# Optimization experiments

Hardware: AMD Instinct MI355X
Metric: run time of the kernel (lower is better)

Reference implementation:

```python
import math
import jax, jax.numpy as jnp
import numpy as np

HID, NHEADS, MEM, LIM = 1024, 16, 512, 2048
HEAD = HID // NHEADS  # 64


def _skew(X, pad_value):
    # shift row m right by m steps: [B, M, L] -> [B, M, M+L]
    B, M, L = X.shape
    X = jnp.pad(X, ((0, 0), (0, 0), (0, M + 1)), constant_values=pad_value)
    X = X.reshape(B, -1)[:, :-M]
    return X.reshape(B, M, M + L)


def _unskew(X):
    # reverse of _skew: [B, M, M+L] -> [B, M, L]
    B, M, LM = X.shape
    L = LM - M
    X = jnp.pad(X.reshape(B, -1), ((0, 0), (0, M)))
    return X.reshape(B, M, LM + 1)[:, :, :L]


def _heads(x):
    # [B, S, K*D] -> [B*K, S, D]
    B, S, _ = x.shape
    return x.reshape(B, S, NHEADS, HEAD).transpose(0, 2, 1, 3).reshape(B * NHEADS, S, HEAD)


def setup_inputs() -> dict:
    key = jax.random.key(0)
    ks = jax.random.split(key, 8)
    B = 8
    s = 1.0 / math.sqrt(HID)
    return {
        "query": jax.random.normal(ks[0], (B, MEM, HID), jnp.float32),
        "key": jax.random.normal(ks[1], (B, MEM + LIM, HID), jnp.float32),
        "value": jax.random.normal(ks[2], (B, MEM + LIM, HID), jnp.float32),
        "key_pe": jax.random.normal(ks[3], (1, HEAD, LIM), jnp.float32),
        "Wq": jax.random.normal(ks[4], (HID, HID), jnp.float32) * s,
        "Wk": jax.random.normal(ks[5], (HID, HID), jnp.float32) * s,
        "Wv": jax.random.normal(ks[6], (HID, HID), jnp.float32) * s,
        "Wo": jax.random.normal(ks[7], (HID, HID), jnp.float32) * s,
    }


def reference(query, key, value, key_pe, Wq, Wk, Wv, Wo):
    B = query.shape[0]
    q = _heads(query @ Wq.T)   # [B*K, M, D]
    k = _heads(key @ Wk.T)     # [B*K, M+L, D]
    v = _heads(value @ Wv.T)   # [B*K, M+L, D]
    # content term via skew/unskew trick
    attn_cont = _unskew(jnp.einsum('bmd,bnd->bmn', q, k))  # [B*K, M, L]
    # relative-position term
    attn_pos = jnp.einsum('bmd,dl->bml', q, key_pe[0])     # [B*K, M, L]
    attn = jax.nn.softmax((attn_cont + attn_pos) / math.sqrt(HEAD), axis=-1)
    out = jnp.matmul(_skew(attn, 0.0), v)                  # [B*K, M, D]
    out = out.reshape(B, NHEADS, MEM, HEAD).transpose(0, 2, 1, 3).reshape(B, MEM, HID)
    return out @ Wo.T
```

## Files before the change

kernel.cpp:

```cpp
#include <hip/hip_runtime.h>
#include <hip/hip_bf16.h>
#include <stdint.h>


typedef __attribute__((ext_vector_type(8))) __bf16 bfrag;
typedef __attribute__((ext_vector_type(4))) float f4;

#define DEVFN static __device__ __forceinline__

DEVFN void glds16(const void* g, void* l) {
  __builtin_amdgcn_global_load_lds((const __attribute__((address_space(1))) void*)g,
                                   (__attribute__((address_space(3))) void*)l, 16, 0, 0);
}

DEVFN bfrag cvt8(const float* p) {
  f4 a = *(const f4*)p;
  f4 b = *(const f4*)(p + 4);
  bfrag v;
  v[0] = (__bf16)a.x; v[1] = (__bf16)a.y; v[2] = (__bf16)a.z; v[3] = (__bf16)a.w;
  v[4] = (__bf16)b.x; v[5] = (__bf16)b.y; v[6] = (__bf16)b.z; v[7] = (__bf16)b.w;
  return v;
}

__global__ __launch_bounds__(256) void conv4(const float* __restrict__ a0, const float* __restrict__ a1,
                                             const float* __restrict__ a2, const float* __restrict__ a3,
                                             __bf16* __restrict__ d0, __bf16* __restrict__ d1,
                                             __bf16* __restrict__ d2, __bf16* __restrict__ d3) {
  int bx = blockIdx.x;
  int sel = bx >> 9;
  const float* s = sel == 0 ? a0 : sel == 1 ? a1 : sel == 2 ? a2 : a3;
  __bf16* d = sel == 0 ? d0 : sel == 1 ? d1 : sel == 2 ? d2 : d3;
  int i = ((bx & 511) * 256 + (int)threadIdx.x) * 8;
  *(bfrag*)(d + i) = cvt8(s + i);
}

__global__ __launch_bounds__(256) void convin(const float* __restrict__ q, const float* __restrict__ k,
                                              const float* __restrict__ v,
                                              __bf16* __restrict__ qd, __bf16* __restrict__ kd,
                                              __bf16* __restrict__ vd) {
  int bx = blockIdx.x;
  const float* s; __bf16* d; int lb;
  if (bx < 2048)       { s = q; d = qd; lb = bx; }
  else if (bx < 12288) { s = k; d = kd; lb = bx - 2048; }
  else                 { s = v; d = vd; lb = bx - 12288; }
  int i = (lb * 256 + (int)threadIdx.x) * 8;
  *(bfrag*)(d + i) = cvt8(s + i);
}

__global__ __launch_bounds__(256) void pek(const float* __restrict__ pe,
                                           __bf16* __restrict__ peT) {
  int i = blockIdx.x * 256 + threadIdx.x;
  if (i < 64 * 2048) {
    int d = i >> 11, l = i & 2047;
    peT[(size_t)(l + 64) * 64 + d] = (__bf16)pe[i];
  } else {
    int zi = i - 64 * 2048;
    int row = zi >> 6, dd = zi & 63;
    int r = row < 64 ? row : (2112 + row - 64);
    peT[(size_t)r * 64 + dd] = (__bf16)0.f;
  }
}

DEVFN bfrag rdfrag(const __bf16* L, int row, int kc, int g) {
  return *(const bfrag*)&L[row * 64 + (((g + 4 * kc) ^ (row & 7)) << 3)];
}

DEVFN void core16(const __bf16* __restrict__ A, const __bf16* __restrict__ B,
                  __bf16* AL, __bf16* BL, f4 (&acc)[4][4],
                  int tid, int wr, int wc, int g, int cl) {
  auto stageA = [&](int s, int k0) {
#pragma unroll
    for (int j = 0; j < 4; ++j) {
      int slot = j * 256 + tid;
      int row = slot >> 3, ch = slot & 7;
      glds16(A + (size_t)row * 1024 + k0 + ((ch ^ (row & 7)) << 3),
             &AL[s * 8192 + (slot << 3)]);
    }
  };
  auto stageB = [&](int k0) {
#pragma unroll
    for (int j = 0; j < 4; ++j) {
      int slot = j * 256 + tid;
      int row = slot >> 3, ch = slot & 7;
      glds16(B + (size_t)row * 1024 + k0 + ((ch ^ (row & 7)) << 3),
             &BL[slot << 3]);
    }
  };

  stageA(0, 0);
  for (int kt = 0; kt < 16; ++kt) {
    const int s = kt & 1;
    stageB(kt * 64);
    if (kt < 15) {
      stageA(s ^ 1, (kt + 1) * 64);
      asm volatile("s_waitcnt vmcnt(4)" ::: "memory");
    } else {
      asm volatile("s_waitcnt vmcnt(0)" ::: "memory");
    }
    __builtin_amdgcn_s_barrier();
    const __bf16* As = &AL[s * 8192];
#pragma unroll
    for (int kc = 0; kc < 2; ++kc) {
      bfrag af[4], bf[4];
#pragma unroll
      for (int i = 0; i < 4; ++i) {
        af[i] = rdfrag(As, 64 * wr + 16 * i + cl, kc, g);
        bf[i] = rdfrag(BL, 64 * wc + 16 * i + cl, kc, g);
      }
      __builtin_amdgcn_s_setprio(1);
#pragma unroll
      for (int am = 0; am < 4; ++am)
#pragma unroll
        for (int bn = 0; bn < 4; ++bn)
          acc[am][bn] =
              __builtin_amdgcn_mfma_f32_16x16x32_bf16(af[am], bf[bn], acc[am][bn], 0, 0, 0);
      __builtin_amdgcn_s_setprio(0);
    }
    __builtin_amdgcn_s_barrier();
  }
}

__global__ __launch_bounds__(256) void projk_c(const __bf16* __restrict__ Aq, const __bf16* __restrict__ Ak,
                                               const __bf16* __restrict__ Av,
                                               const __bf16* __restrict__ Wqb, const __bf16* __restrict__ Wkb,
                                               const __bf16* __restrict__ Wvb,
                                               __bf16* __restrict__ qws, __bf16* __restrict__ kws,
                                               __bf16* __restrict__ vtws) {
  __shared__ alignas(16) __bf16 AL[2 * 128 * 64];
  __shared__ alignas(16) __bf16 BL[128 * 64];
  int bx = blockIdx.x;
  const __bf16* A; const __bf16* B; __bf16* C; int nb, lb, rpb, trans;
  if (bx < 256)       { A = Aq; B = Wqb; C = qws;  lb = bx;        nb = 256;  rpb = 4;  trans = 0; }
  else if (bx < 1536) { A = Ak; B = Wkb; C = kws;  lb = bx - 256;  nb = 1280; rpb = 20; trans = 0; }
  else                { A = Av; B = Wvb; C = vtws; lb = bx - 1536; nb = 1280; rpb = 20; trans = 1; }

  const int tid = threadIdx.x;
  const int lane = tid & 63, wv = tid >> 6;
  const int wr = wv >> 1, wc = wv & 1;
  const int g = lane >> 4, cl = lane & 15;

  int v = (lb & 7) * (nb >> 3) + (lb >> 3);
  const int trow = v >> 3;
  const int r0 = trow * 128, c0 = (v & 7) * 128;

  f4 acc[4][4] = {};
  core16(A + (size_t)r0 * 1024, B + (size_t)c0 * 1024, AL, BL, acc,
         tid, wr, wc, g, cl);

  int Sseq = rpb << 7;
  int b = trow / rpb;
  int sbase = r0 - b * Sseq;
#pragma unroll
  for (int am = 0; am < 4; ++am)
#pragma unroll
    for (int bn = 0; bn < 4; ++bn) {
      int jg = c0 + 64 * wc + 16 * bn + cl;
      int h = jg >> 6, d = jg & 63;
#pragma unroll
      for (int r = 0; r < 4; ++r) {
        int s = sbase + 64 * wr + 16 * am + 4 * g + r;
        size_t dst = trans ? ((size_t)(b * 16 + h) * 64 + d) * 2560 + s
                           : ((size_t)(b * 16 + h) * Sseq + s) * 64 + d;
        C[dst] = (__bf16)acc[am][bn][r];
      }
    }
}

DEVFN void stageA_row(const float* ap, __bf16* lds, int arow, int ahalf) {
  const f4* p = (const f4*)ap;
#pragma unroll
  for (int q = 0; q < 4; ++q) {
    f4 a = p[2 * q], b = p[2 * q + 1];
    bfrag v;
    v[0] = (__bf16)a.x; v[1] = (__bf16)a.y; v[2] = (__bf16)a.z; v[3] = (__bf16)a.w;
    v[4] = (__bf16)b.x; v[5] = (__bf16)b.y; v[6] = (__bf16)b.z; v[7] = (__bf16)b.w;
    int ch = (4 * ahalf + q) ^ (arow & 7);
    *(bfrag*)&lds[arow * 64 + ch * 8] = v;
  }
}

__global__ __launch_bounds__(256) void projk_f32(const float* __restrict__ Aq, const float* __restrict__ Ak,
                                                 const float* __restrict__ Av,
                                                 const __bf16* __restrict__ Wqb, const __bf16* __restrict__ Wkb,
                                                 const __bf16* __restrict__ Wvb,
                                                 __bf16* __restrict__ qws, __bf16* __restrict__ kws,
                                                 __bf16* __restrict__ vtws) {
  __shared__ alignas(16) __bf16 Alds[128 * 64];
  __shared__ alignas(16) __bf16 Blds[128 * 64];
  int bx = blockIdx.x;
  const float* A; const __bf16* B; __bf16* C; int nb, lb, rpb, trans;
  if (bx < 256)       { A = Aq; B = Wqb; C = qws;  lb = bx;        nb = 256;  rpb = 4;  trans = 0; }
  else if (bx < 1536) { A = Ak; B = Wkb; C = kws;  lb = bx - 256;  nb = 1280; rpb = 20; trans = 0; }
  else                { A = Av; B = Wvb; C = vtws; lb = bx - 1536; nb = 1280; rpb = 20; trans = 1; }

  const int tid = threadIdx.x;
  const int lane = tid & 63, wv = tid >> 6;
  const int wr = wv >> 1, wc = wv & 1;
  const int g = lane >> 4, cl = lane & 15;

  int v = (lb & 7) * (nb >> 3) + (lb >> 3);
  const int trow = v >> 3;
  const int r0 = trow * 128, c0 = (v & 7) * 128;

  f4 acc[4][4] = {};

  for (int k0 = 0; k0 < 1024; k0 += 64) {
    __syncthreads();
#pragma unroll
    for (int i = 0; i < 4; ++i) {
      int slot = tid + 256 * i;
      int row = slot >> 3, ch = slot & 7;
      glds16(B + (size_t)(c0 + row) * 1024 + k0 + ((ch ^ (row & 7)) << 3),
             &Blds[slot << 3]);
    }
    stageA_row(A + (size_t)(r0 + (tid >> 1)) * 1024 + k0 + (tid & 1) * 32,
               Alds, tid >> 1, tid & 1);
    __syncthreads();
#pragma unroll
    for (int kc = 0; kc < 2; ++kc) {
      bfrag af[4], bfv[4];
#pragma unroll
      for (int i = 0; i < 4; ++i) {
        int rA = 64 * wr + 16 * i + cl;
        af[i] = *(const bfrag*)&Alds[rA * 64 + (((g + 4 * kc) ^ (rA & 7)) << 3)];
        int rB = 64 * wc + 16 * i + cl;
        bfv[i] = *(const bfrag*)&Blds[rB * 64 + (((g + 4 * kc) ^ (rB & 7)) << 3)];
      }
#pragma unroll
      for (int am = 0; am < 4; ++am)
#pragma unroll
        for (int bn = 0; bn < 4; ++bn)
          acc[am][bn] =
              __builtin_amdgcn_mfma_f32_16x16x32_bf16(af[am], bfv[bn], acc[am][bn], 0, 0, 0);
    }
  }

  int Sseq = rpb << 7;
  int b = trow / rpb;
  int sbase = r0 - b * Sseq;
#pragma unroll
  for (int am = 0; am < 4; ++am)
#pragma unroll
    for (int bn = 0; bn < 4; ++bn) {
      int jg = c0 + 64 * wc + 16 * bn + cl;
      int h = jg >> 6, d = jg & 63;
#pragma unroll
      for (int r = 0; r < 4; ++r) {
        int s = sbase + 64 * wr + 16 * am + 4 * g + r;
        size_t dst = trans ? ((size_t)(b * 16 + h) * 64 + d) * 2560 + s
                           : ((size_t)(b * 16 + h) * Sseq + s) * 64 + d;
        C[dst] = (__bf16)acc[am][bn][r];
      }
    }
}

__global__ __launch_bounds__(256) void gemm_out(const __bf16* __restrict__ A,
                                                const __bf16* __restrict__ B,
                                                float* __restrict__ C) {
  __shared__ alignas(16) __bf16 AL[2 * 128 * 64];
  __shared__ alignas(16) __bf16 BL[128 * 64];
  const int tid = threadIdx.x;
  const int lane = tid & 63, wv = tid >> 6;
  const int wr = wv >> 1, wc = wv & 1;
  const int g = lane >> 4, cl = lane & 15;

  int bx = blockIdx.x;
  int v = (bx & 7) * 32 + (bx >> 3);
  const int r0 = (v >> 3) * 128, c0 = (v & 7) * 128;

  f4 acc[4][4] = {};
  core16(A + (size_t)r0 * 1024, B + (size_t)c0 * 1024, AL, BL, acc,
         tid, wr, wc, g, cl);

#pragma unroll
  for (int am = 0; am < 4; ++am)
#pragma unroll
    for (int bn = 0; bn < 4; ++bn)
#pragma unroll
      for (int r = 0; r < 4; ++r) {
        int rg = r0 + 64 * wr + 16 * am + 4 * g + r;
        int jg = c0 + 64 * wc + 16 * bn + cl;
        C[(size_t)rg * 1024 + jg] = acc[am][bn][r];
      }
}

#define SCL 0.18033688011112042f
#define FMX 20.0f

__global__ __launch_bounds__(256) void attnk(const __bf16* __restrict__ qws,
                                             const __bf16* __restrict__ kws,
                                             const __bf16* __restrict__ vtws,
                                             const __bf16* __restrict__ pews,
                                             __bf16* __restrict__ obuf) {
  __shared__ alignas(16) __bf16 Ks[64 * 64];
  __shared__ alignas(16) __bf16 QVs[64 * 64];
  __shared__ alignas(16) __bf16 PPs[64 * 64];
  __shared__ alignas(16) __bf16 Pbs[64 * 128];

  int bx = blockIdx.x;
  int vv = (bx & 7) * 128 + (bx >> 3);
  int bh = vv >> 3, mt = vv & 7;
  int m0 = mt * 64;
  const __bf16* qb = qws + (size_t)bh * 512 * 64;
  const __bf16* kb = kws + (size_t)bh * 2560 * 64;
  const __bf16* vb = vtws + (size_t)bh * 64 * 2560;

  const int tid = threadIdx.x;
  const int lane = tid & 63, w = tid >> 6;
  const int g = lane >> 4, cl = lane & 15;

#pragma unroll
  for (int i = 0; i < 2; ++i) {
    int slot = tid + 256 * i;
    int row = slot >> 3, ch = slot & 7;
    glds16(qb + (size_t)(m0 + row) * 64 + ((ch ^ (row & 7)) << 3), &QVs[slot << 3]);
  }
  __syncthreads();
  bfrag qf_all[4][2];
#pragma unroll
  for (int rb = 0; rb < 4; ++rb) {
    int rq = 16 * rb + cl;
#pragma unroll
    for (int kc = 0; kc < 2; ++kc)
      qf_all[rb][kc] = *(const bfrag*)&QVs[rq * 64 + (((g + 4 * kc) ^ (rq & 7)) << 3)];
  }

  f4 o[4] = {};
  float lsum[4] = {};

  for (int t = 0; t < 33; ++t) {
    int n0 = m0 + 64 * t;
    __syncthreads();
#pragma unroll
    for (int i = 0; i < 2; ++i) {
      int slot = tid + 256 * i;
      int row = slot >> 3, ch = slot & 7;
      glds16(kb + (size_t)(n0 + row) * 64 + ((ch ^ (row & 7)) << 3), &Ks[slot << 3]);
      glds16(vb + (size_t)row * 2560 + n0 + ((ch ^ (row & 7)) << 3), &QVs[slot << 3]);
      glds16(pews + (size_t)(64 * (t + 1) + row) * 64 + ((ch ^ (row & 7)) << 3),
             &PPs[slot << 3]);
    }
    __syncthreads();

    f4 sc[4] = {};
    __builtin_amdgcn_s_setprio(1);
#pragma unroll
    for (int kc = 0; kc < 2; ++kc)
#pragma unroll
      for (int cb = 0; cb < 4; ++cb) {
        int rk = 16 * cb + cl;
        bfrag kf = *(const bfrag*)&Ks[rk * 64 + (((g + 4 * kc) ^ (rk & 7)) << 3)];
        sc[cb] = __builtin_amdgcn_mfma_f32_16x16x32_bf16(qf_all[w][kc], kf, sc[cb], 0, 0, 0);
      }
    f4 pbacc[4] = {};
#pragma unroll
    for (int kc = 0; kc < 2; ++kc) {
      int rp = 16 * w + cl;
      bfrag pf = *(const bfrag*)&PPs[rp * 64 + (((g + 4 * kc) ^ (rp & 7)) << 3)];
#pragma unroll
      for (int rb = 0; rb < 4; ++rb)
        pbacc[rb] = __builtin_amdgcn_mfma_f32_16x16x32_bf16(qf_all[rb][kc], pf, pbacc[rb], 0, 0, 0);
    }
    __builtin_amdgcn_s_setprio(0);
    {
      int half = (t & 1) << 6;
      int c2 = 16 * w + cl;
#pragma unroll
      for (int rb = 0; rb < 4; ++rb)
#pragma unroll
        for (int r = 0; r < 4; ++r)
          Pbs[(16 * rb + 4 * g + r) * 128 + half + c2] = (__bf16)pbacc[rb][r];
    }
    __syncthreads();

    bool edge = (t == 0) || (t == 32);
#pragma unroll
    for (int r = 0; r < 4; ++r) {
      int jm = 16 * w + 4 * g + r;
#pragma unroll
      for (int cb = 0; cb < 4; ++cb) {
        int jn = 16 * cb + cl;
        int l = 64 * t + jn - jm;
        float pv = (float)Pbs[jm * 128 + (l & 127)];
        float ex = fmaf(sc[cb][r] + pv, SCL, -FMX);
        if (edge) ex = ((unsigned)l < 2048u) ? ex : -1e30f;
        float p = __builtin_amdgcn_exp2f(ex);
        lsum[r] += p;
        PPs[jm * 64 + (((jn >> 3) ^ (jm & 7)) << 3) + (jn & 7)] = (__bf16)p;
      }
    }

    __builtin_amdgcn_s_setprio(1);
#pragma unroll
    for (int kc = 0; kc < 2; ++kc) {
      int rp2 = 16 * w + cl;
      bfrag pa = *(const bfrag*)&PPs[rp2 * 64 + (((g + 4 * kc) ^ (rp2 & 7)) << 3)];
#pragma unroll
      for (int cb = 0; cb < 4; ++cb) {
        int rv = 16 * cb + cl;
        bfrag vf = *(const bfrag*)&QVs[rv * 64 + (((g + 4 * kc) ^ (rv & 7)) << 3)];
        o[cb] = __builtin_amdgcn_mfma_f32_16x16x32_bf16(pa, vf, o[cb], 0, 0, 0);
      }
    }
    __builtin_amdgcn_s_setprio(0);
  }

#pragma unroll
  for (int r = 0; r < 4; ++r)
#pragma unroll
    for (int off = 1; off < 16; off <<= 1) lsum[r] += __shfl_xor(lsum[r], off);

  int b = bh >> 4, h = bh & 15;
#pragma unroll
  for (int cb = 0; cb < 4; ++cb)
#pragma unroll
    for (int r = 0; r < 4; ++r) {
      int m = m0 + 16 * w + 4 * g + r;
      int d = 16 * cb + cl;
      obuf[((size_t)(b * 512 + m)) * 1024 + h * 64 + d] = (__bf16)(o[cb][r] / lsum[r]);
    }
}

extern "C" void kernel_launch(void* const* d_in, const int* in_sizes, int n_in,
                              void* d_out, int out_size, void* d_ws, size_t ws_size,
                              hipStream_t stream) {
  const float* query = (const float*)d_in[0];
  const float* key   = (const float*)d_in[1];
  const float* value = (const float*)d_in[2];
  const float* keype = (const float*)d_in[3];
  const float* Wq    = (const float*)d_in[4];
  const float* Wk    = (const float*)d_in[5];
  const float* Wv    = (const float*)d_in[6];
  const float* Wo    = (const float*)d_in[7];
  float* out = (float*)d_out;
  (void)in_sizes; (void)n_in; (void)out_size;

  char* ws = (char*)d_ws;
  size_t off = 0;
  auto alloc = [&](size_t bytes) {
    void* p = ws + off;
    off += (bytes + 255) & ~(size_t)255;
    return p;
  };
  __bf16* Wqb  = (__bf16*)alloc((size_t)1024 * 1024 * 2);
  __bf16* Wkb  = (__bf16*)alloc((size_t)1024 * 1024 * 2);
  __bf16* Wvb  = (__bf16*)alloc((size_t)1024 * 1024 * 2);
  __bf16* Wob  = (__bf16*)alloc((size_t)1024 * 1024 * 2);
  __bf16* peT  = (__bf16*)alloc((size_t)2176 * 64 * 2);
  __bf16* qws  = (__bf16*)alloc((size_t)128 * 512 * 64 * 2);
  __bf16* kws  = (__bf16*)alloc((size_t)128 * 2560 * 64 * 2);
  __bf16* vtws = (__bf16*)alloc((size_t)128 * 2560 * 64 * 2);

  const size_t NEED = (size_t)194 * 1024 * 1024;
  bool big = ws_size >= NEED;

  conv4<<<2048, 256, 0, stream>>>(Wq, Wk, Wv, Wo, Wqb, Wkb, Wvb, Wob);
  pek<<<544, 256, 0, stream>>>(keype, peT);

  __bf16* obuf;
  if (big) {
    __bf16* qbf = (__bf16*)alloc((size_t)8 * 512 * 1024 * 2);
    __bf16* kbf = (__bf16*)alloc((size_t)8 * 2560 * 1024 * 2);
    __bf16* vbf = (__bf16*)alloc((size_t)8 * 2560 * 1024 * 2);
    obuf = qbf;
    convin<<<22528, 256, 0, stream>>>(query, key, value, qbf, kbf, vbf);
    projk_c<<<2816, 256, 0, stream>>>(qbf, kbf, vbf, Wqb, Wkb, Wvb, qws, kws, vtws);
  } else {
    obuf = (__bf16*)alloc((size_t)4096 * 1024 * 2);
    projk_f32<<<2816, 256, 0, stream>>>(query, key, value, Wqb, Wkb, Wvb,
                                        qws, kws, vtws);
  }

  attnk<<<1024, 256, 0, stream>>>(qws, kws, vtws, peT, obuf);
  gemm_out<<<256, 256, 0, stream>>>(obuf, Wob, out);
}
```

Measured before the change: 379.9 us.

## Keep attention probabilities in registers and transpose score MFMA layout

```diff
diff --git a/kernel.cpp b/kernel.cpp
--- a/kernel.cpp
+++ b/kernel.cpp
@@ -5,6 +5,7 @@
 
 typedef __attribute__((ext_vector_type(8))) __bf16 bfrag;
 typedef __attribute__((ext_vector_type(4))) float f4;
+typedef __attribute__((ext_vector_type(4))) unsigned int u32x4;
 
 #define DEVFN static __device__ __forceinline__
 
@@ -20,6 +21,21 @@
   v[0] = (__bf16)a.x; v[1] = (__bf16)a.y; v[2] = (__bf16)a.z; v[3] = (__bf16)a.w;
   v[4] = (__bf16)b.x; v[5] = (__bf16)b.y; v[6] = (__bf16)b.z; v[7] = (__bf16)b.w;
   return v;
+}
+
+DEVFN uint32_t cvtpk(float lo, float hi) {
+  uint32_t r;
+  asm("v_cvt_pk_bf16_f32 %0, %1, %2" : "=v"(r) : "v"(lo), "v"(hi));
+  return r;
+}
+
+DEVFN uint32_t bperm(int addr, uint32_t v) {
+  return (uint32_t)__builtin_amdgcn_ds_bpermute(addr, (int)v);
+}
+
+DEVFN bfrag as_bfrag(uint32_t a, uint32_t b, uint32_t c, uint32_t d) {
+  u32x4 t = {a, b, c, d};
+  return __builtin_bit_cast(bfrag, t);
 }
 
 __global__ __launch_bounds__(256) void conv4(const float* __restrict__ a0, const float* __restrict__ a1,
@@ -293,9 +309,8 @@
                                              const __bf16* __restrict__ pews,
                                              __bf16* __restrict__ obuf) {
   __shared__ alignas(16) __bf16 Ks[64 * 64];
-  __shared__ alignas(16) __bf16 QVs[64 * 64];
-  __shared__ alignas(16) __bf16 PPs[64 * 64];
-  __shared__ alignas(16) __bf16 Pbs[64 * 128];
+  __shared__ alignas(16) __bf16 Vs[64 * 64];
+  __shared__ alignas(16) __bf16 ring[64 * 132];
 
   int bx = blockIdx.x;
   int vv = (bx & 7) * 128 + (bx >> 3);
@@ -309,115 +324,124 @@
   const int lane = tid & 63, w = tid >> 6;
   const int g = lane >> 4, cl = lane & 15;
 
-#pragma unroll
-  for (int i = 0; i < 2; ++i) {
-    int slot = tid + 256 * i;
-    int row = slot >> 3, ch = slot & 7;
-    glds16(qb + (size_t)(m0 + row) * 64 + ((ch ^ (row & 7)) << 3), &QVs[slot << 3]);
-  }
-  __syncthreads();
-  bfrag qf_all[4][2];
-#pragma unroll
-  for (int rb = 0; rb < 4; ++rb) {
-    int rq = 16 * rb + cl;
-#pragma unroll
-    for (int kc = 0; kc < 2; ++kc)
-      qf_all[rb][kc] = *(const bfrag*)&QVs[rq * 64 + (((g + 4 * kc) ^ (rq & 7)) << 3)];
-  }
+  bfrag qf[2];
+  {
+    const __bf16* qrow = qb + (size_t)(m0 + 16 * w + cl) * 64 + 8 * g;
+    qf[0] = *(const bfrag*)qrow;
+    qf[1] = *(const bfrag*)(qrow + 32);
+  }
+
+  const int addrA = (32 * (g & 1) + cl) * 4;
+  const int addrB = addrA + 64;
+  const bool hi = (g >> 1) != 0;
+  const int rowoff = (16 * w + cl) * 132;
 
   f4 o[4] = {};
-  float lsum[4] = {};
+  float lsum = 0.f;
 
   for (int t = 0; t < 33; ++t) {
     int n0 = m0 + 64 * t;
     __syncthreads();
+
+    bfrag pef[4][2];
+    {
+      const __bf16* peb = pews + (size_t)(64 + 64 * t + cl) * 64 + 8 * g;
+#pragma unroll
+      for (int lb = 0; lb < 4; ++lb) {
+        pef[lb][0] = *(const bfrag*)(peb + (size_t)(16 * lb) * 64);
+        pef[lb][1] = *(const bfrag*)(peb + (size_t)(16 * lb) * 64 + 32);
+      }
+    }
 #pragma unroll
     for (int i = 0; i < 2; ++i) {
       int slot = tid + 256 * i;
       int row = slot >> 3, ch = slot & 7;
       glds16(kb + (size_t)(n0 + row) * 64 + ((ch ^ (row & 7)) << 3), &Ks[slot << 3]);
-      glds16(vb + (size_t)row * 2560 + n0 + ((ch ^ (row & 7)) << 3), &QVs[slot << 3]);
-      glds16(pews + (size_t)(64 * (t + 1) + row) * 64 + ((ch ^ (row & 7)) << 3),
-             &PPs[slot << 3]);
+      glds16(vb + (size_t)row * 2560 + n0 + ((ch ^ (row & 7)) << 3), &Vs[slot << 3]);
+    }
+
+#pragma unroll
+    for (int lb = 0; lb < 4; ++lb) {
+      f4 pbv = {};
+      pbv = __builtin_amdgcn_mfma_f32_16x16x32_bf16(pef[lb][0], qf[0], pbv, 0, 0, 0);
+      pbv = __builtin_amdgcn_mfma_f32_16x16x32_bf16(pef[lb][1], qf[1], pbv, 0, 0, 0);
+      int colbase = (64 * t + 16 * lb + 4 * g) & 127;
+      *(uint32_t*)&ring[rowoff + colbase]     = cvtpk(pbv[0], pbv[1]);
+      *(uint32_t*)&ring[rowoff + colbase + 2] = cvtpk(pbv[2], pbv[3]);
     }
     __syncthreads();
 
     f4 sc[4] = {};
     __builtin_amdgcn_s_setprio(1);
 #pragma unroll
-    for (int kc = 0; kc < 2; ++kc)
-#pragma unroll
-      for (int cb = 0; cb < 4; ++cb) {
-        int rk = 16 * cb + cl;
-        bfrag kf = *(const bfrag*)&Ks[rk * 64 + (((g + 4 * kc) ^ (rk & 7)) << 3)];
-        sc[cb] = __builtin_amdgcn_mfma_f32_16x16x32_bf16(qf_all[w][kc], kf, sc[cb], 0, 0, 0);
-      }
-    f4 pbacc[4] = {};
+    for (int nb = 0; nb < 4; ++nb) {
+      bfrag kf0 = rdfrag(Ks, 16 * nb + cl, 0, g);
+      sc[nb] = __builtin_amdgcn_mfma_f32_16x16x32_bf16(kf0, qf[0], sc[nb], 0, 0, 0);
+      bfrag kf1 = rdfrag(Ks, 16 * nb + cl, 1, g);
+      sc[nb] = __builtin_amdgcn_mfma_f32_16x16x32_bf16(kf1, qf[1], sc[nb], 0, 0, 0);
+    }
+    __builtin_amdgcn_s_setprio(0);
+
+    bool edge = (t == 0) | (t == 32);
+    float p[4][4];
+    int l0 = 64 * t + 4 * g - cl - 16 * w;
+#pragma unroll
+    for (int nb = 0; nb < 4; ++nb)
+#pragma unroll
+      for (int r = 0; r < 4; ++r) {
+        int l = l0 + 16 * nb + r;
+        float pv = (float)ring[rowoff + (l & 127)];
+        float ex = fmaf(sc[nb][r] + pv, SCL, -FMX);
+        if (edge) ex = ((unsigned)l < 2048u) ? ex : -1e30f;
+        float pp = __builtin_amdgcn_exp2f(ex);
+        lsum += pp;
+        p[nb][r] = pp;
+      }
+    uint32_t pk[4][2];
+#pragma unroll
+    for (int nb = 0; nb < 4; ++nb) {
+      pk[nb][0] = cvtpk(p[nb][0], p[nb][1]);
+      pk[nb][1] = cvtpk(p[nb][2], p[nb][3]);
+    }
+
+    __builtin_amdgcn_s_setprio(1);
 #pragma unroll
     for (int kc = 0; kc < 2; ++kc) {
-      int rp = 16 * w + cl;
-      bfrag pf = *(const bfrag*)&PPs[rp * 64 + (((g + 4 * kc) ^ (rp & 7)) << 3)];
-#pragma unroll
-      for (int rb = 0; rb < 4; ++rb)
-        pbacc[rb] = __builtin_amdgcn_mfma_f32_16x16x32_bf16(qf_all[rb][kc], pf, pbacc[rb], 0, 0, 0);
+      uint32_t t0, t1, u0, u1, u2, u3;
+      t0 = bperm(addrA, pk[2 * kc][0]); t1 = bperm(addrA, pk[2 * kc + 1][0]);
+      u0 = hi ? t1 : t0;
+      t0 = bperm(addrA, pk[2 * kc][1]); t1 = bperm(addrA, pk[2 * kc + 1][1]);
+      u1 = hi ? t1 : t0;
+      t0 = bperm(addrB, pk[2 * kc][0]); t1 = bperm(addrB, pk[2 * kc + 1][0]);
+      u2 = hi ? t1 : t0;
+      t0 = bperm(addrB, pk[2 * kc][1]); t1 = bperm(addrB, pk[2 * kc + 1][1]);
+      u3 = hi ? t1 : t0;
+      bfrag pa = as_bfrag(u0, u1, u2, u3);
+#pragma unroll
+      for (int db = 0; db < 4; ++db) {
+        bfrag vf = rdfrag(Vs, 16 * db + cl, kc, g);
+        o[db] = __builtin_amdgcn_mfma_f32_16x16x32_bf16(pa, vf, o[db], 0, 0, 0);
+      }
     }
     __builtin_amdgcn_s_setprio(0);
-    {
-      int half = (t & 1) << 6;
-      int c2 = 16 * w + cl;
-#pragma unroll
-      for (int rb = 0; rb < 4; ++rb)
-#pragma unroll
-        for (int r = 0; r < 4; ++r)
-          Pbs[(16 * rb + 4 * g + r) * 128 + half + c2] = (__bf16)pbacc[rb][r];
-    }
-    __syncthreads();
-
-    bool edge = (t == 0) || (t == 32);
-#pragma unroll
-    for (int r = 0; r < 4; ++r) {
-      int jm = 16 * w + 4 * g + r;
-#pragma unroll
-      for (int cb = 0; cb < 4; ++cb) {
-        int jn = 16 * cb + cl;
-        int l = 64 * t + jn - jm;
-        float pv = (float)Pbs[jm * 128 + (l & 127)];
-        float ex = fmaf(sc[cb][r] + pv, SCL, -FMX);
-        if (edge) ex = ((unsigned)l < 2048u) ? ex : -1e30f;
-        float p = __builtin_amdgcn_exp2f(ex);
-        lsum[r] += p;
-        PPs[jm * 64 + (((jn >> 3) ^ (jm & 7)) << 3) + (jn & 7)] = (__bf16)p;
-      }
-    }
-
-    __builtin_amdgcn_s_setprio(1);
-#pragma unroll
-    for (int kc = 0; kc < 2; ++kc) {
-      int rp2 = 16 * w + cl;
-      bfrag pa = *(const bfrag*)&PPs[rp2 * 64 + (((g + 4 * kc) ^ (rp2 & 7)) << 3)];
-#pragma unroll
-      for (int cb = 0; cb < 4; ++cb) {
-        int rv = 16 * cb + cl;
-        bfrag vf = *(const bfrag*)&QVs[rv * 64 + (((g + 4 * kc) ^ (rv & 7)) << 3)];
-        o[cb] = __builtin_amdgcn_mfma_f32_16x16x32_bf16(pa, vf, o[cb], 0, 0, 0);
-      }
-    }
-    __builtin_amdgcn_s_setprio(0);
-  }
-
+  }
+
+  lsum += __shfl_xor(lsum, 16);
+  lsum += __shfl_xor(lsum, 32);
+  float rinv = 1.f / lsum;
+  float rv[4];
 #pragma unroll
   for (int r = 0; r < 4; ++r)
-#pragma unroll
-    for (int off = 1; off < 16; off <<= 1) lsum[r] += __shfl_xor(lsum[r], off);
+    rv[r] = __shfl(rinv, 4 * g + r);
 
   int b = bh >> 4, h = bh & 15;
 #pragma unroll
-  for (int cb = 0; cb < 4; ++cb)
+  for (int db = 0; db < 4; ++db)
 #pragma unroll
     for (int r = 0; r < 4; ++r) {
       int m = m0 + 16 * w + 4 * g + r;
-      int d = 16 * cb + cl;
-      obuf[((size_t)(b * 512 + m)) * 1024 + h * 64 + d] = (__bf16)(o[cb][r] / lsum[r]);
+      int d = 16 * db + cl;
+      obuf[((size_t)(b * 512 + m)) * 1024 + h * 64 + d] = (__bf16)(o[db][r] * rv[r]);
     }
 }
 
```

Result: no change. 383.1 us (+0.8%).
